# Kernel tuning notes

Measured on AMD Instinct MI355X. Metric: run time of the kernel, lower is better.

## Reference

```python
import jax, jax.numpy as jnp
import numpy as np

NEG_SLOPE = 0.2  # PyG GATConv default negative_slope


def gat_conv(x, src, dst, W, a_src, a_dst, b, concat):
    """One GATConv layer (PyG semantics, self-loops already included in src/dst).

    x: [N, F_in]; src, dst: [E] int; W: [F_in, H*C]; a_src, a_dst: [H, C]; b: bias.
    """
    N = x.shape[0]
    H, C = a_src.shape
    h = (x @ W).reshape(N, H, C)                      # projected node features
    alpha_src = jnp.sum(h * a_src, axis=-1)           # [N, H]
    alpha_dst = jnp.sum(h * a_dst, axis=-1)           # [N, H]
    logits = jax.nn.leaky_relu(alpha_src[src] + alpha_dst[dst], NEG_SLOPE)  # [E, H]
    # softmax over incoming edges of each destination node (numerically stable)
    m = jax.ops.segment_max(logits, dst, num_segments=N)                    # [N, H]
    p = jnp.exp(logits - m[dst])
    denom = jax.ops.segment_sum(p, dst, num_segments=N)                     # [N, H]
    alpha = p / denom[dst]                                                  # [E, H]
    # attention-weighted scatter-add aggregation
    out = jax.ops.segment_sum(alpha[:, :, None] * h[src], dst, num_segments=N)  # [N, H, C]
    out = out.reshape(N, H * C) if concat else out.mean(axis=1)
    return out + b


def setup_inputs() -> dict:
    key = jax.random.key(0)
    ks = jax.random.split(key, 10)
    N, E = 50000, 800000
    nfeats, hidden, nclasses, in_head, out_head = 256, 32, 40, 8, 1
    s = 0.05
    return {
        "x": jax.random.normal(ks[0], (N, nfeats), dtype=jnp.float32),
        "edge_index": jax.random.randint(ks[1], (2, E), 0, N, dtype=jnp.int32),
        "w1": jax.random.normal(ks[2], (nfeats, in_head * hidden), dtype=jnp.float32) * s,
        "a_src1": jax.random.normal(ks[3], (in_head, hidden), dtype=jnp.float32) * s,
        "a_dst1": jax.random.normal(ks[4], (in_head, hidden), dtype=jnp.float32) * s,
        "b1": jnp.zeros((in_head * hidden,), dtype=jnp.float32),
        "w2": jax.random.normal(ks[5], (in_head * hidden, out_head * nclasses), dtype=jnp.float32) * s,
        "a_src2": jax.random.normal(ks[6], (out_head, nclasses), dtype=jnp.float32) * s,
        "a_dst2": jax.random.normal(ks[7], (out_head, nclasses), dtype=jnp.float32) * s,
        "b2": jnp.zeros((nclasses,), dtype=jnp.float32),
    }


def reference(x, edge_index, w1, a_src1, a_dst1, b1, w2, a_src2, a_dst2, b2):
    N = x.shape[0]
    loops = jnp.arange(N, dtype=edge_index.dtype)
    src = jnp.concatenate([edge_index[0], loops])  # PyG add_self_loops=True
    dst = jnp.concatenate([edge_index[1], loops])
    h = gat_conv(x, src, dst, w1, a_src1, a_dst1, b1, concat=True)
    h = jax.nn.elu(h)
    out = gat_conv(h, src, dst, w2, a_src2, a_dst2, b2, concat=False)
    return out
```

## Files before the change

kernel.cpp:

```cpp
#include <hip/hip_runtime.h>
#include <cstdint>
#include <cstddef>

constexpr int Nn   = 50000;
constexpr int Ee   = 800000;
constexpr int ETot = Ee + Nn;
constexpr int H1   = 8;
constexpr int C1h  = 32;
constexpr int HC1  = 256;
constexpr int C2   = 40;
constexpr int S2   = 64;
constexpr float SLOPE = 0.2f;
constexpr int NB_SCAN = (Nn + 255) / 256;

typedef __attribute__((ext_vector_type(8))) short bf16x8;
typedef __attribute__((ext_vector_type(4))) float f32x4;

__device__ __forceinline__ ushort f2bf(float f) {
    uint u = __float_as_uint(f);
    u += 0x7fffu + ((u >> 16) & 1u);
    return (ushort)(u >> 16);
}
__device__ __forceinline__ float bf2f(ushort b) {
    return __uint_as_float(((uint)b) << 16);
}

__device__ __forceinline__ void gload16(const void* g, void* lds) {
    typedef const __attribute__((address_space(1))) unsigned int GU;
    typedef __attribute__((address_space(3))) unsigned int LU;
    __builtin_amdgcn_global_load_lds((GU*)g, (LU*)lds, 16, 0, 0);
}

__global__ void k_prep(const float* __restrict__ x, ushort* __restrict__ xhi,
                       ushort* __restrict__ xlo, const float* __restrict__ w1,
                       ushort* __restrict__ WT2, const float* __restrict__ w2,
                       ushort* __restrict__ WT2b, const int* __restrict__ dstA,
                       int* __restrict__ counts) {
    int t = blockIdx.x * blockDim.x + threadIdx.x;
    constexpr int n4 = Nn * HC1 / 4;
    if (t < n4) {
        float4 v = *(const float4*)(x + (size_t)t * 4);
        ushort4 h, l;
        h.x = f2bf(v.x); l.x = f2bf(v.x - bf2f(h.x));
        h.y = f2bf(v.y); l.y = f2bf(v.y - bf2f(h.y));
        h.z = f2bf(v.z); l.z = f2bf(v.z - bf2f(h.z));
        h.w = f2bf(v.w); l.w = f2bf(v.w - bf2f(h.w));
        *(ushort4*)(xhi + (size_t)t * 4) = h;
        *(ushort4*)(xlo + (size_t)t * 4) = l;
    }
    if (t < ETot) {
        int d = (t < Ee) ? dstA[t] : t - Ee;
        atomicAdd(&counts[d], 1);
    }
    if (t < 256 * 256) {
        int k = t >> 8, col = t & 255;
        float w = w1[(size_t)k * 256 + col];
        ushort h = f2bf(w), l = f2bf(w - bf2f(h));
        int kb = k >> 3, kr = k & 7;
        WT2[((size_t)(kb)      * 256 + col) * 8 + kr] = h;
        WT2[((size_t)(kb + 32) * 256 + col) * 8 + kr] = h;
        WT2[((size_t)(kb + 64) * 256 + col) * 8 + kr] = l;
    }
    if (t < 256 * 48) {
        int k = t / 48, col = t % 48;
        float w = (col < C2) ? w2[(size_t)k * C2 + col] : 0.f;
        ushort h = f2bf(w), l = f2bf(w - bf2f(h));
        int kb = k >> 3, kr = k & 7;
        WT2b[((size_t)(kb)      * 48 + col) * 8 + kr] = h;
        WT2b[((size_t)(kb + 32) * 48 + col) * 8 + kr] = h;
        WT2b[((size_t)(kb + 64) * 48 + col) * 8 + kr] = l;
    }
}

__global__ __launch_bounds__(256) void k_scan_block(const int* __restrict__ counts,
                                                    int* __restrict__ exsc,
                                                    int* __restrict__ bsum) {
    __shared__ int sm[256];
    int i = blockIdx.x * 256 + threadIdx.x;
    int v = (i < Nn) ? counts[i] : 0;
    sm[threadIdx.x] = v;
    __syncthreads();
#pragma unroll
    for (int off = 1; off < 256; off <<= 1) {
        int t = (threadIdx.x >= off) ? sm[threadIdx.x - off] : 0;
        __syncthreads();
        sm[threadIdx.x] += t;
        __syncthreads();
    }
    if (i < Nn) exsc[i] = sm[threadIdx.x] - v;
    if (threadIdx.x == 255) bsum[blockIdx.x] = sm[255];
}

__global__ __launch_bounds__(256) void k_finalize2(const int* __restrict__ exsc,
                                                   const int* __restrict__ bsum,
                                                   int* __restrict__ row_off,
                                                   int* __restrict__ cursor) {
    __shared__ int sm[256];
    int t = threadIdx.x;
    int v = (t < NB_SCAN) ? bsum[t] : 0;
    sm[t] = v;
    __syncthreads();
#pragma unroll
    for (int off = 1; off < 256; off <<= 1) {
        int x = (t >= off) ? sm[t - off] : 0;
        __syncthreads();
        sm[t] += x;
        __syncthreads();
    }
    int i = blockIdx.x * 256 + t;
    if (i < Nn) {
        int r = exsc[i] + sm[blockIdx.x] - bsum[blockIdx.x];
        row_off[i] = r;
        cursor[i] = r;
    }
    if (i == 0) row_off[Nn] = ETot;
}

__global__ void k_scatter(const int* __restrict__ srcA, const int* __restrict__ dstA,
                          int* __restrict__ cursor, int* __restrict__ csr_src) {
    int e = blockIdx.x * blockDim.x + threadIdx.x;
    if (e >= ETot) return;
    int s, d;
    if (e < Ee) { s = srcA[e]; d = dstA[e]; } else { s = e - Ee; d = s; }
    int pos = atomicAdd(&cursor[d], 1);
    csr_src[pos] = s;
}

__global__ __launch_bounds__(256, 4) void k_gemm1_mfma(const ushort* __restrict__ xhi,
                                                       const ushort* __restrict__ xlo,
                                                       const ushort* __restrict__ WT2,
                                                       ushort* __restrict__ h1b,
                                                       const float* __restrict__ a_s,
                                                       const float* __restrict__ a_d,
                                                       float* __restrict__ asrc1,
                                                       float* __restrict__ adst1, int M) {
    constexpr int BK = 32, KD = 768;
    __shared__ __align__(16) ushort As[2][64 * BK];
    __shared__ __align__(16) ushort Bs[2][256 * BK];
    const int tid = threadIdx.x;
    const int bm = blockIdx.x * 64;
    const int lane = tid & 63;
    const int w = tid >> 6;
    const int l16 = lane & 15, lk = lane >> 4;

    const int sakc = tid >> 6, sarow = tid & 63;
    int arow = bm + sarow; arow = arow < M ? arow : M - 1;

    auto stage = [&](int buf, int k0) {
        const ushort* xsec; int ks;
        if (k0 < 256)      { xsec = xhi; ks = k0; }
        else if (k0 < 512) { xsec = xlo; ks = k0 - 256; }
        else               { xsec = xhi; ks = k0 - 512; }
        gload16(xsec + (size_t)arow * 256 + ks + sakc * 8, As[buf] + tid * 8);
        const ushort* bbase = WT2 + (size_t)(k0 >> 3) * 256 * 8;
#pragma unroll
        for (int q = 0; q < 4; q++)
            gload16(bbase + (size_t)(q * 256 + tid) * 8, Bs[buf] + (q * 256 + tid) * 8);
    };

    f32x4 acc[4][4] = {};
    stage(0, 0);
    __syncthreads();
    int buf = 0;
    for (int k0 = 0; k0 < KD; k0 += BK) {
        if (k0 + BK < KD) stage(buf ^ 1, k0 + BK);
        bf16x8 a[4], b[4];
#pragma unroll
        for (int m = 0; m < 4; m++)
            a[m] = *(const bf16x8*)(As[buf] + (lk * 64 + m * 16 + l16) * 8);
#pragma unroll
        for (int n = 0; n < 4; n++)
            b[n] = *(const bf16x8*)(Bs[buf] + (lk * 256 + w * 64 + n * 16 + l16) * 8);
#pragma unroll
        for (int m = 0; m < 4; m++)
#pragma unroll
            for (int n = 0; n < 4; n++)
                acc[m][n] = __builtin_amdgcn_mfma_f32_16x16x32_bf16(a[m], b[n], acc[m][n], 0, 0, 0);
        __syncthreads();
        buf ^= 1;
    }
    float as_v[4], ad_v[4];
#pragma unroll
    for (int n = 0; n < 4; n++) {
        int col = w * 64 + n * 16 + l16;
        as_v[n] = a_s[col];
        ad_v[n] = a_d[col];
    }
#pragma unroll
    for (int m = 0; m < 4; m++) {
#pragma unroll
        for (int j = 0; j < 4; j++) {
            int row = bm + m * 16 + lk * 4 + j;
            float ps0 = acc[m][0][j] * as_v[0] + acc[m][1][j] * as_v[1];
            float ps1 = acc[m][2][j] * as_v[2] + acc[m][3][j] * as_v[3];
            float pd0 = acc[m][0][j] * ad_v[0] + acc[m][1][j] * ad_v[1];
            float pd1 = acc[m][2][j] * ad_v[2] + acc[m][3][j] * ad_v[3];
#pragma unroll
            for (int off = 1; off < 16; off <<= 1) {
                ps0 += __shfl_xor(ps0, off);
                ps1 += __shfl_xor(ps1, off);
                pd0 += __shfl_xor(pd0, off);
                pd1 += __shfl_xor(pd1, off);
            }
            if (row < M) {
#pragma unroll
                for (int n = 0; n < 4; n++)
                    h1b[(size_t)row * 256 + w * 64 + n * 16 + l16] = f2bf(acc[m][n][j]);
                if (l16 == 0) {
                    asrc1[(size_t)row * H1 + w * 2]     = ps0;
                    asrc1[(size_t)row * H1 + w * 2 + 1] = ps1;
                    adst1[(size_t)row * H1 + w * 2]     = pd0;
                    adst1[(size_t)row * H1 + w * 2 + 1] = pd1;
                }
            }
        }
    }
}

__global__ __launch_bounds__(256, 4) void k_gemm2_mfma(const ushort* __restrict__ hi,
                                                       const ushort* __restrict__ lo,
                                                       const ushort* __restrict__ WT,
                                                       ushort* __restrict__ h2,
                                                       const float* __restrict__ a_s,
                                                       const float* __restrict__ a_d,
                                                       float* __restrict__ asrc2,
                                                       float* __restrict__ adst2, int M) {
    constexpr int BK = 32, KD = 768;
    __shared__ __align__(16) ushort As[2][64 * BK];
    __shared__ __align__(16) ushort Bs[2][48 * BK];
    const int tid = threadIdx.x;
    const int bm = blockIdx.x * 64;
    const int lane = tid & 63;
    const int w = tid >> 6;
    const int l16 = lane & 15, lk = lane >> 4;

    const int sakc = tid >> 6, sarow = tid & 63;
    int arow = bm + sarow; arow = arow < M ? arow : M - 1;

    auto stage = [&](int buf, int k0) {
        const ushort* xsec; int ks;
        if (k0 < 256)      { xsec = hi; ks = k0; }
        else if (k0 < 512) { xsec = lo; ks = k0 - 256; }
        else               { xsec = hi; ks = k0 - 512; }
        gload16(xsec + (size_t)arow * 256 + ks + sakc * 8, As[buf] + tid * 8);
        if (tid < 192)
            gload16(WT + ((size_t)(k0 >> 3) * 48 + tid) * 8, Bs[buf] + tid * 8);
    };

    f32x4 acc[3] = {};
    stage(0, 0);
    __syncthreads();
    int buf = 0;
    for (int k0 = 0; k0 < KD; k0 += BK) {
        if (k0 + BK < KD) stage(buf ^ 1, k0 + BK);
        bf16x8 a2, b2[3];
        a2 = *(const bf16x8*)(As[buf] + (lk * 64 + w * 16 + l16) * 8);
#pragma unroll
        for (int n = 0; n < 3; n++)
            b2[n] = *(const bf16x8*)(Bs[buf] + (lk * 48 + n * 16 + l16) * 8);
#pragma unroll
        for (int n = 0; n < 3; n++)
            acc[n] = __builtin_amdgcn_mfma_f32_16x16x32_bf16(a2, b2[n], acc[n], 0, 0, 0);
        __syncthreads();
        buf ^= 1;
    }
    float asv[3], adv[3];
#pragma unroll
    for (int n = 0; n < 3; n++) {
        int col = n * 16 + l16;
        asv[n] = (col < C2) ? a_s[col] : 0.f;
        adv[n] = (col < C2) ? a_d[col] : 0.f;
    }
#pragma unroll
    for (int j = 0; j < 4; j++) {
        int row = bm + w * 16 + lk * 4 + j;
        float ps = acc[0][j] * asv[0] + acc[1][j] * asv[1] + acc[2][j] * asv[2];
        float pd = acc[0][j] * adv[0] + acc[1][j] * adv[1] + acc[2][j] * adv[2];
#pragma unroll
        for (int off = 1; off < 16; off <<= 1) {
            ps += __shfl_xor(ps, off);
            pd += __shfl_xor(pd, off);
        }
        if (row < M) {
#pragma unroll
            for (int n = 0; n < 3; n++)
                h2[(size_t)row * S2 + n * 16 + l16] = f2bf(acc[n][j]);
            if (l16 == 0) { asrc2[row] = ps; adst2[row] = pd; }
        }
    }
}

__global__ __launch_bounds__(256) void k_gat_aggr1(const int* __restrict__ row_off,
                                                   const int* __restrict__ csr_src,
                                                   const float* __restrict__ asrc,
                                                   const float* __restrict__ adst,
                                                   const ushort* __restrict__ h1b,
                                                   const float* __restrict__ bias,
                                                   ushort* __restrict__ o_hi,
                                                   ushort* __restrict__ o_lo) {
    int wid = (blockIdx.x * 256 + threadIdx.x) >> 6;
    if (wid >= Nn) return;
    int lane = threadIdx.x & 63;
    int half = lane >> 5, l32 = lane & 31;
    int head = l32 >> 2;
    int c0 = l32 * 8;
    int beg = row_off[wid], end = row_off[wid + 1];
    float ad = adst[(size_t)wid * H1 + head];
    float acc[8] = {};
    float sump = 0.f;
    int i = beg + half;
    for (; i + 6 < end; i += 8) {
        int s0 = csr_src[i],     s1 = csr_src[i + 2];
        int s2 = csr_src[i + 4], s3 = csr_src[i + 6];
        float a0 = asrc[(size_t)s0 * H1 + head], a1 = asrc[(size_t)s1 * H1 + head];
        float a2 = asrc[(size_t)s2 * H1 + head], a3 = asrc[(size_t)s3 * H1 + head];
        bf16x8 v0 = *(const bf16x8*)(h1b + (size_t)s0 * HC1 + c0);
        bf16x8 v1 = *(const bf16x8*)(h1b + (size_t)s1 * HC1 + c0);
        bf16x8 v2 = *(const bf16x8*)(h1b + (size_t)s2 * HC1 + c0);
        bf16x8 v3 = *(const bf16x8*)(h1b + (size_t)s3 * HC1 + c0);
        float l0 = a0 + ad; l0 = l0 > 0.f ? l0 : SLOPE * l0;
        float l1 = a1 + ad; l1 = l1 > 0.f ? l1 : SLOPE * l1;
        float l2 = a2 + ad; l2 = l2 > 0.f ? l2 : SLOPE * l2;
        float l3 = a3 + ad; l3 = l3 > 0.f ? l3 : SLOPE * l3;
        float p0 = __expf(l0), p1 = __expf(l1), p2 = __expf(l2), p3 = __expf(l3);
        sump += (p0 + p1) + (p2 + p3);
#pragma unroll
        for (int j = 0; j < 8; j++)
            acc[j] += (p0 * bf2f((ushort)v0[j]) + p1 * bf2f((ushort)v1[j])) +
                      (p2 * bf2f((ushort)v2[j]) + p3 * bf2f((ushort)v3[j]));
    }
    for (; i < end; i += 2) {
        int s = csr_src[i];
        float a = asrc[(size_t)s * H1 + head];
        bf16x8 v = *(const bf16x8*)(h1b + (size_t)s * HC1 + c0);
        float l = a + ad; l = l > 0.f ? l : SLOPE * l;
        float p = __expf(l);
        sump += p;
#pragma unroll
        for (int j = 0; j < 8; j++) acc[j] += p * bf2f((ushort)v[j]);
    }
    sump += __shfl_xor(sump, 32);
#pragma unroll
    for (int j = 0; j < 8; j++) acc[j] += __shfl_xor(acc[j], 32);
    if (half) return;
    float inv = 1.f / sump;
    float4 b0 = *(const float4*)(bias + c0);
    float4 b1 = *(const float4*)(bias + c0 + 4);
    float bb[8] = {b0.x, b0.y, b0.z, b0.w, b1.x, b1.y, b1.z, b1.w};
    uint4 uh, ul;
    uint* uhp = (uint*)&uh; uint* ulp = (uint*)&ul;
#pragma unroll
    for (int q = 0; q < 4; q++) {
        float r0 = acc[2 * q] * inv + bb[2 * q];
        float r1 = acc[2 * q + 1] * inv + bb[2 * q + 1];
        r0 = r0 > 0.f ? r0 : __expf(r0) - 1.f;
        r1 = r1 > 0.f ? r1 : __expf(r1) - 1.f;
        ushort h0 = f2bf(r0), h1v = f2bf(r1);
        ushort l0 = f2bf(r0 - bf2f(h0)), l1v = f2bf(r1 - bf2f(h1v));
        uhp[q] = (uint)h0 | ((uint)h1v << 16);
        ulp[q] = (uint)l0 | ((uint)l1v << 16);
    }
    *(uint4*)(o_hi + (size_t)wid * HC1 + c0) = uh;
    *(uint4*)(o_lo + (size_t)wid * HC1 + c0) = ul;
}

__global__ __launch_bounds__(256) void k_gat_aggr2(const int* __restrict__ row_off,
                                                   const int* __restrict__ csr_src,
                                                   const float* __restrict__ asrc,
                                                   const float* __restrict__ adst,
                                                   const ushort* __restrict__ h2,
                                                   const float* __restrict__ bias,
                                                   float* __restrict__ out) {
    int wid = (blockIdx.x * 256 + threadIdx.x) >> 6;
    if (wid >= Nn) return;
    int lane = threadIdx.x & 63;
    int cl = lane < C2 ? lane : C2 - 1;
    int beg = row_off[wid], end = row_off[wid + 1];
    float ad = adst[wid];
    float acc = 0.f, sump = 0.f;
    int i = beg;
    for (; i + 3 < end; i += 4) {
        int s0 = csr_src[i], s1 = csr_src[i + 1], s2 = csr_src[i + 2], s3 = csr_src[i + 3];
        float a0 = asrc[s0], a1 = asrc[s1], a2 = asrc[s2], a3 = asrc[s3];
        float v0 = bf2f(h2[(size_t)s0 * S2 + cl]);
        float v1 = bf2f(h2[(size_t)s1 * S2 + cl]);
        float v2 = bf2f(h2[(size_t)s2 * S2 + cl]);
        float v3 = bf2f(h2[(size_t)s3 * S2 + cl]);
        float l0 = a0 + ad; l0 = l0 > 0.f ? l0 : SLOPE * l0;
        float l1 = a1 + ad; l1 = l1 > 0.f ? l1 : SLOPE * l1;
        float l2 = a2 + ad; l2 = l2 > 0.f ? l2 : SLOPE * l2;
        float l3 = a3 + ad; l3 = l3 > 0.f ? l3 : SLOPE * l3;
        float p0 = __expf(l0), p1 = __expf(l1), p2 = __expf(l2), p3 = __expf(l3);
        sump += (p0 + p1) + (p2 + p3);
        acc += p0 * v0 + p1 * v1 + p2 * v2 + p3 * v3;
    }
    for (; i < end; i++) {
        int s = csr_src[i];
        float l = asrc[s] + ad;
        l = l > 0.f ? l : SLOPE * l;
        float pe = __expf(l);
        sump += pe;
        acc += pe * bf2f(h2[(size_t)s * S2 + cl]);
    }
    if (lane < C2) out[(size_t)wid * C2 + lane] = acc / sump + bias[lane];
}

extern "C" void kernel_launch(void* const* d_in, const int* in_sizes, int n_in,
                              void* d_out, int out_size, void* d_ws, size_t ws_size,
                              hipStream_t stream) {
    const float* x   = (const float*)d_in[0];
    const int*   ei  = (const int*)d_in[1];
    const float* w1  = (const float*)d_in[2];
    const float* as1 = (const float*)d_in[3];
    const float* ad1 = (const float*)d_in[4];
    const float* b1  = (const float*)d_in[5];
    const float* w2  = (const float*)d_in[6];
    const float* as2 = (const float*)d_in[7];
    const float* ad2 = (const float*)d_in[8];
    const float* b2  = (const float*)d_in[9];
    float* outp = (float*)d_out;

    const int* srcA = ei;
    const int* dstA = ei + Ee;

    char* W = (char*)d_ws;
    size_t o = 0;
    auto allocB = [&](size_t bytes) { void* p = W + o; o += (bytes + 255) & ~(size_t)255; return p; };

    ushort* xhi   = (ushort*)allocB((size_t)Nn * HC1 * 2);
    ushort* xlo   = (ushort*)allocB((size_t)Nn * HC1 * 2);
    ushort* o1hi  = xhi;
    ushort* o1lo  = xlo;
    ushort* wt2   = (ushort*)allocB((size_t)768 * 256 * 2);
    ushort* wt2b  = (ushort*)allocB((size_t)768 * 48 * 2);
    ushort* h1b   = (ushort*)allocB((size_t)Nn * HC1 * 2);
    ushort* h2    = (ushort*)allocB((size_t)Nn * S2 * 2);
    float*  asrc1 = (float*)allocB((size_t)Nn * H1 * 4);
    float*  adst1 = (float*)allocB((size_t)Nn * H1 * 4);
    float*  asrc2 = (float*)allocB((size_t)Nn * 4);
    float*  adst2 = (float*)allocB((size_t)Nn * 4);
    int* counts   = (int*)allocB((size_t)Nn * 4);
    int* exsc     = (int*)allocB((size_t)Nn * 4);
    int* bsum     = (int*)allocB(256 * 4);
    int* row_off  = (int*)allocB((size_t)(Nn + 1) * 4);
    int* cursor   = (int*)allocB((size_t)Nn * 4);
    int* csr_src  = (int*)allocB((size_t)ETot * 4);

    hipMemsetAsync(counts, 0, (size_t)Nn * sizeof(int), stream);
    k_prep<<<(Nn * HC1 / 4 + 255) / 256, 256, 0, stream>>>(
        x, xhi, xlo, w1, wt2, w2, wt2b, dstA, counts);

    k_scan_block<<<NB_SCAN, 256, 0, stream>>>(counts, exsc, bsum);
    k_finalize2<<<NB_SCAN, 256, 0, stream>>>(exsc, bsum, row_off, cursor);
    k_scatter<<<(ETot + 255) / 256, 256, 0, stream>>>(srcA, dstA, cursor, csr_src);

    k_gemm1_mfma<<<(Nn + 63) / 64, 256, 0, stream>>>(
        xhi, xlo, wt2, h1b, as1, ad1, asrc1, adst1, Nn);
    k_gat_aggr1<<<(int)(((size_t)Nn * 64 + 255) / 256), 256, 0, stream>>>(
        row_off, csr_src, asrc1, adst1, h1b, b1, o1hi, o1lo);

    k_gemm2_mfma<<<(Nn + 63) / 64, 256, 0, stream>>>(
        o1hi, o1lo, wt2b, h2, as2, ad2, asrc2, adst2, Nn);
    k_gat_aggr2<<<(int)(((size_t)Nn * 64 + 255) / 256), 256, 0, stream>>>(
        row_off, csr_src, asrc2, adst2, h2, b2, outp);
}
```

Before: 285.2 us.

## Restructure split-bf16 GEMMs to read B from global and halve aggr2 waves

Both GEMM kernels stop staging the weight tiles in shared memory. B fragments are now read straight from global or L2, and the split-precision loop runs hi*hi over the first 8 steps plus a hi*lo pass, then lo*hi over the last 8. The weight layout drops the duplicated hi copy, shrinking it from 768 to 512 k-rows, and gemm1's launch bounds drop from 4 to 3 waves. The second aggregation kernel now packs two destination nodes per wave, with each lane handling two channels via 32-bit loads, so idle lanes are cut. The risks are higher global-memory latency on the B reads without LDS reuse, and register pressure from the changed occupancy hint.

Result: faster. 273.9 us (-4.0%).

```diff
diff --git a/kernel.cpp b/kernel.cpp
--- a/kernel.cpp
+++ b/kernel.cpp
@@ -58,8 +58,7 @@
         ushort h = f2bf(w), l = f2bf(w - bf2f(h));
         int kb = k >> 3, kr = k & 7;
         WT2[((size_t)(kb)      * 256 + col) * 8 + kr] = h;
-        WT2[((size_t)(kb + 32) * 256 + col) * 8 + kr] = h;
-        WT2[((size_t)(kb + 64) * 256 + col) * 8 + kr] = l;
+        WT2[((size_t)(kb + 32) * 256 + col) * 8 + kr] = l;
     }
     if (t < 256 * 48) {
         int k = t / 48, col = t % 48;
@@ -67,8 +66,7 @@
         ushort h = f2bf(w), l = f2bf(w - bf2f(h));
         int kb = k >> 3, kr = k & 7;
         WT2b[((size_t)(kb)      * 48 + col) * 8 + kr] = h;
-        WT2b[((size_t)(kb + 32) * 48 + col) * 8 + kr] = h;
-        WT2b[((size_t)(kb + 64) * 48 + col) * 8 + kr] = l;
+        WT2b[((size_t)(kb + 32) * 48 + col) * 8 + kr] = l;
     }
 }
 
@@ -126,7 +124,7 @@
     csr_src[pos] = s;
 }
 
-__global__ __launch_bounds__(256, 4) void k_gemm1_mfma(const ushort* __restrict__ xhi,
+__global__ __launch_bounds__(256, 3) void k_gemm1_mfma(const ushort* __restrict__ xhi,
                                                        const ushort* __restrict__ xlo,
                                                        const ushort* __restrict__ WT2,
                                                        ushort* __restrict__ h1b,
@@ -134,9 +132,7 @@
                                                        const float* __restrict__ a_d,
                                                        float* __restrict__ asrc1,
                                                        float* __restrict__ adst1, int M) {
-    constexpr int BK = 32, KD = 768;
-    __shared__ __align__(16) ushort As[2][64 * BK];
-    __shared__ __align__(16) ushort Bs[2][256 * BK];
+    __shared__ __align__(16) ushort As[2][64 * 32];
     const int tid = threadIdx.x;
     const int bm = blockIdx.x * 64;
     const int lane = tid & 63;
@@ -146,36 +142,45 @@
     const int sakc = tid >> 6, sarow = tid & 63;
     int arow = bm + sarow; arow = arow < M ? arow : M - 1;
 
-    auto stage = [&](int buf, int k0) {
-        const ushort* xsec; int ks;
-        if (k0 < 256)      { xsec = xhi; ks = k0; }
-        else if (k0 < 512) { xsec = xlo; ks = k0 - 256; }
-        else               { xsec = xhi; ks = k0 - 512; }
+    auto stageA = [&](int buf, int t) {
+        const ushort* xsec = (t < 8) ? xhi : xlo;
+        int ks = (t & 7) * 32;
         gload16(xsec + (size_t)arow * 256 + ks + sakc * 8, As[buf] + tid * 8);
-        const ushort* bbase = WT2 + (size_t)(k0 >> 3) * 256 * 8;
-#pragma unroll
-        for (int q = 0; q < 4; q++)
-            gload16(bbase + (size_t)(q * 256 + tid) * 8, Bs[buf] + (q * 256 + tid) * 8);
     };
 
     f32x4 acc[4][4] = {};
-    stage(0, 0);
+    stageA(0, 0);
     __syncthreads();
     int buf = 0;
-    for (int k0 = 0; k0 < KD; k0 += BK) {
-        if (k0 + BK < KD) stage(buf ^ 1, k0 + BK);
-        bf16x8 a[4], b[4];
+    for (int t = 0; t < 16; t++) {
+        if (t + 1 < 16) stageA(buf ^ 1, t + 1);
+        int kc = t & 7;
+        bf16x8 a[4];
 #pragma unroll
         for (int m = 0; m < 4; m++)
             a[m] = *(const bf16x8*)(As[buf] + (lk * 64 + m * 16 + l16) * 8);
+        bf16x8 bh[4];
 #pragma unroll
         for (int n = 0; n < 4; n++)
-            b[n] = *(const bf16x8*)(Bs[buf] + (lk * 256 + w * 64 + n * 16 + l16) * 8);
+            bh[n] = *(const bf16x8*)(WT2 +
+                ((size_t)(kc * 4 + lk) * 256 + w * 64 + n * 16 + l16) * 8);
 #pragma unroll
         for (int m = 0; m < 4; m++)
 #pragma unroll
             for (int n = 0; n < 4; n++)
-                acc[m][n] = __builtin_amdgcn_mfma_f32_16x16x32_bf16(a[m], b[n], acc[m][n], 0, 0, 0);
+                acc[m][n] = __builtin_amdgcn_mfma_f32_16x16x32_bf16(a[m], bh[n], acc[m][n], 0, 0, 0);
+        if (t < 8) {
+            bf16x8 bl[4];
+#pragma unroll
+            for (int n = 0; n < 4; n++)
+                bl[n] = *(const bf16x8*)(WT2 +
+                    ((size_t)(32 + kc * 4 + lk) * 256 + w * 64 + n * 16 + l16) * 8);
+#pragma unroll
+            for (int m = 0; m < 4; m++)
+#pragma unroll
+                for (int n = 0; n < 4; n++)
+                    acc[m][n] = __builtin_amdgcn_mfma_f32_16x16x32_bf16(a[m], bl[n], acc[m][n], 0, 0, 0);
+        }
         __syncthreads();
         buf ^= 1;
     }
@@ -225,9 +230,7 @@
                                                        const float* __restrict__ a_d,
                                                        float* __restrict__ asrc2,
                                                        float* __restrict__ adst2, int M) {
-    constexpr int BK = 32, KD = 768;
-    __shared__ __align__(16) ushort As[2][64 * BK];
-    __shared__ __align__(16) ushort Bs[2][48 * BK];
+    __shared__ __align__(16) ushort As[2][64 * 32];
     const int tid = threadIdx.x;
     const int bm = blockIdx.x * 64;
     const int lane = tid & 63;
@@ -237,30 +240,38 @@
     const int sakc = tid >> 6, sarow = tid & 63;
     int arow = bm + sarow; arow = arow < M ? arow : M - 1;
 
-    auto stage = [&](int buf, int k0) {
-        const ushort* xsec; int ks;
-        if (k0 < 256)      { xsec = hi; ks = k0; }
-        else if (k0 < 512) { xsec = lo; ks = k0 - 256; }
-        else               { xsec = hi; ks = k0 - 512; }
+    auto stageA = [&](int buf, int t) {
+        const ushort* xsec = (t < 8) ? hi : lo;
+        int ks = (t & 7) * 32;
         gload16(xsec + (size_t)arow * 256 + ks + sakc * 8, As[buf] + tid * 8);
-        if (tid < 192)
-            gload16(WT + ((size_t)(k0 >> 3) * 48 + tid) * 8, Bs[buf] + tid * 8);
     };
 
     f32x4 acc[3] = {};
-    stage(0, 0);
+    stageA(0, 0);
     __syncthreads();
     int buf = 0;
-    for (int k0 = 0; k0 < KD; k0 += BK) {
-        if (k0 + BK < KD) stage(buf ^ 1, k0 + BK);
-        bf16x8 a2, b2[3];
-        a2 = *(const bf16x8*)(As[buf] + (lk * 64 + w * 16 + l16) * 8);
+    for (int t = 0; t < 16; t++) {
+        if (t + 1 < 16) stageA(buf ^ 1, t + 1);
+        int kc = t & 7;
+        bf16x8 a2 = *(const bf16x8*)(As[buf] + (lk * 64 + w * 16 + l16) * 8);
+        bf16x8 bh[3];
 #pragma unroll
         for (int n = 0; n < 3; n++)
-            b2[n] = *(const bf16x8*)(Bs[buf] + (lk * 48 + n * 16 + l16) * 8);
+            bh[n] = *(const bf16x8*)(WT +
+                ((size_t)(kc * 4 + lk) * 48 + n * 16 + l16) * 8);
 #pragma unroll
         for (int n = 0; n < 3; n++)
-            acc[n] = __builtin_amdgcn_mfma_f32_16x16x32_bf16(a2, b2[n], acc[n], 0, 0, 0);
+            acc[n] = __builtin_amdgcn_mfma_f32_16x16x32_bf16(a2, bh[n], acc[n], 0, 0, 0);
+        if (t < 8) {
+            bf16x8 bl[3];
+#pragma unroll
+            for (int n = 0; n < 3; n++)
+                bl[n] = *(const bf16x8*)(WT +
+                    ((size_t)(32 + kc * 4 + lk) * 48 + n * 16 + l16) * 8);
+#pragma unroll
+            for (int n = 0; n < 3; n++)
+                acc[n] = __builtin_amdgcn_mfma_f32_16x16x32_bf16(a2, bl[n], acc[n], 0, 0, 0);
+        }
         __syncthreads();
         buf ^= 1;
     }
@@ -371,28 +382,33 @@
                                                    const ushort* __restrict__ h2,
                                                    const float* __restrict__ bias,
                                                    float* __restrict__ out) {
-    int wid = (blockIdx.x * 256 + threadIdx.x) >> 6;
+    int gw = (blockIdx.x * 256 + threadIdx.x) >> 6;
+    int lane = threadIdx.x & 63;
+    int half = lane >> 5, l32 = lane & 31;
+    int wid = gw * 2 + half;
     if (wid >= Nn) return;
-    int lane = threadIdx.x & 63;
-    int cl = lane < C2 ? lane : C2 - 1;
+    int c = l32 * 2;
     int beg = row_off[wid], end = row_off[wid + 1];
     float ad = adst[wid];
-    float acc = 0.f, sump = 0.f;
+    float acc0 = 0.f, acc1 = 0.f, sump = 0.f;
     int i = beg;
     for (; i + 3 < end; i += 4) {
         int s0 = csr_src[i], s1 = csr_src[i + 1], s2 = csr_src[i + 2], s3 = csr_src[i + 3];
         float a0 = asrc[s0], a1 = asrc[s1], a2 = asrc[s2], a3 = asrc[s3];
-        float v0 = bf2f(h2[(size_t)s0 * S2 + cl]);
-        float v1 = bf2f(h2[(size_t)s1 * S2 + cl]);
-        float v2 = bf2f(h2[(size_t)s2 * S2 + cl]);
-        float v3 = bf2f(h2[(size_t)s3 * S2 + cl]);
+        uint u0 = *(const uint*)(h2 + (size_t)s0 * S2 + c);
+        uint u1 = *(const uint*)(h2 + (size_t)s1 * S2 + c);
+        uint u2 = *(const uint*)(h2 + (size_t)s2 * S2 + c);
+        uint u3 = *(const uint*)(h2 + (size_t)s3 * S2 + c);
         float l0 = a0 + ad; l0 = l0 > 0.f ? l0 : SLOPE * l0;
         float l1 = a1 + ad; l1 = l1 > 0.f ? l1 : SLOPE * l1;
         float l2 = a2 + ad; l2 = l2 > 0.f ? l2 : SLOPE * l2;
         float l3 = a3 + ad; l3 = l3 > 0.f ? l3 : SLOPE * l3;
         float p0 = __expf(l0), p1 = __expf(l1), p2 = __expf(l2), p3 = __expf(l3);
         sump += (p0 + p1) + (p2 + p3);
-        acc += p0 * v0 + p1 * v1 + p2 * v2 + p3 * v3;
+        acc0 += p0 * bf2f((ushort)(u0 & 0xffff)) + p1 * bf2f((ushort)(u1 & 0xffff)) +
+                p2 * bf2f((ushort)(u2 & 0xffff)) + p3 * bf2f((ushort)(u3 & 0xffff));
+        acc1 += p0 * bf2f((ushort)(u0 >> 16)) + p1 * bf2f((ushort)(u1 >> 16)) +
+                p2 * bf2f((ushort)(u2 >> 16)) + p3 * bf2f((ushort)(u3 >> 16));
     }
     for (; i < end; i++) {
         int s = csr_src[i];
@@ -400,9 +416,17 @@
         l = l > 0.f ? l : SLOPE * l;
         float pe = __expf(l);
         sump += pe;
-        acc += pe * bf2f(h2[(size_t)s * S2 + cl]);
-    }
-    if (lane < C2) out[(size_t)wid * C2 + lane] = acc / sump + bias[lane];
+        uint u = *(const uint*)(h2 + (size_t)s * S2 + c);
+        acc0 += pe * bf2f((ushort)(u & 0xffff));
+        acc1 += pe * bf2f((ushort)(u >> 16));
+    }
+    if (c < C2) {
+        float inv = 1.f / sump;
+        float2 r;
+        r.x = acc0 * inv + bias[c];
+        r.y = acc1 * inv + bias[c + 1];
+        *(float2*)(out + (size_t)wid * C2 + c) = r;
+    }
 }
 
 extern "C" void kernel_launch(void* const* d_in, const int* in_sizes, int n_in,
@@ -431,8 +455,8 @@
     ushort* xlo   = (ushort*)allocB((size_t)Nn * HC1 * 2);
     ushort* o1hi  = xhi;
     ushort* o1lo  = xlo;
-    ushort* wt2   = (ushort*)allocB((size_t)768 * 256 * 2);
-    ushort* wt2b  = (ushort*)allocB((size_t)768 * 48 * 2);
+    ushort* wt2   = (ushort*)allocB((size_t)512 * 256 * 2);
+    ushort* wt2b  = (ushort*)allocB((size_t)512 * 48 * 2);
     ushort* h1b   = (ushort*)allocB((size_t)Nn * HC1 * 2);
     ushort* h2    = (ushort*)allocB((size_t)Nn * S2 * 2);
     float*  asrc1 = (float*)allocB((size_t)Nn * H1 * 4);
@@ -461,6 +485,7 @@
 
     k_gemm2_mfma<<<(Nn + 63) / 64, 256, 0, stream>>>(
         o1hi, o1lo, wt2b, h2, as2, ad2, asrc2, adst2, Nn);
-    k_gat_aggr2<<<(int)(((size_t)Nn * 64 + 255) / 256), 256, 0, stream>>>(
+    int waves2 = (Nn + 1) / 2;
+    k_gat_aggr2<<<(int)(((size_t)waves2 * 64 + 255) / 256), 256, 0, stream>>>(
         row_off, csr_src, asrc2, adst2, h2, b2, outp);
 }
```
